# Performance work log

Hardware: AMD Instinct MI355X
Metric: run time of the kernel (lower is better)

Reference implementation:

```python
import jax, jax.numpy as jnp
import numpy as np
from jax import lax

B, T, D = 4, 1024, 1024
H = 16
HD = D // H
MIN_K, MAX_K = 3, 9
KS = (3, 5, 7, 9)  # candidate odd kernel sizes


def setup_inputs() -> dict:
    key = jax.random.key(0)
    ks = jax.random.split(key, 16)
    s = 0.02
    inp = {
        "x": jax.random.normal(ks[0], (B, T, D), jnp.float32),
        "Wq": jax.random.normal(ks[1], (D, D), jnp.float32) * s,
        "bq": jnp.zeros((D,), jnp.float32),
        "Wk": jax.random.normal(ks[2], (D, D), jnp.float32) * s,
        "bk": jnp.zeros((D,), jnp.float32),
        "Wv": jax.random.normal(ks[3], (D, D), jnp.float32) * s,
        "bv": jnp.zeros((D,), jnp.float32),
        # per-head Conv1d weights (H, out_ch=HD, in_ch=HD, MAX_K) and biases (H, HD)
        "conv_w": jax.random.normal(ks[4], (H, HD, HD, MAX_K), jnp.float32) * s,
        "conv_b": jax.random.normal(ks[5], (H, HD), jnp.float32) * s,
        # kernel_proj: Linear(1,16) -> ReLU -> Linear(16,1), stored as (in,out)
        "kp_w1": jax.random.normal(ks[6], (1, 16), jnp.float32) * 0.5,
        "kp_b1": jnp.zeros((16,), jnp.float32),
        "kp_w2": jax.random.normal(ks[7], (16, 1), jnp.float32) * 0.5,
        "kp_b2": jnp.zeros((1,), jnp.float32),
        "fc_w": jax.random.normal(ks[8], (D, D), jnp.float32) * s,
        "fc_b": jnp.zeros((D,), jnp.float32),
        "ln_g": jnp.ones((D,), jnp.float32),
        "ln_b": jnp.zeros((D,), jnp.float32),
    }
    return inp


def reference(x, Wq, bq, Wk, bk, Wv, bv, conv_w, conv_b,
              kp_w1, kp_b1, kp_w2, kp_b2, fc_w, fc_b, ln_g, ln_b):
    scale = HD ** -0.5
    q = (x @ Wq + bq).reshape(B, T, H, HD).transpose(0, 2, 1, 3)  # (B,H,T,HD)
    k = (x @ Wk + bk).reshape(B, T, H, HD).transpose(0, 2, 1, 3)
    v = (x @ Wv + bv).reshape(B, T, H, HD).transpose(0, 2, 1, 3)

    attn = jax.nn.softmax(jnp.einsum('bhqd,bhkd->bhqk', q, k) * scale, axis=-1)

    # head importance -> dynamic kernel size per head
    importance = attn.mean(axis=(-2, -1)).mean(axis=0)  # (H,)
    imp_norm = (importance - importance.min()) / (importance.max() - importance.min() + 1e-6)
    hmid = jax.nn.relu(imp_norm[:, None] @ kp_w1 + kp_b1)  # (H,16)
    frac = jax.nn.sigmoid((hmid @ kp_w2 + kp_b2)[:, 0])    # (H,)
    kv = jnp.round(MIN_K + frac * (MAX_K - MIN_K)).astype(jnp.int32)
    kv = kv + (1 - kv % 2)                                 # force odd
    kv = jnp.clip(kv, MIN_K, MAX_K)
    k_idx = jnp.clip((kv - MIN_K) // 2, 0, len(KS) - 1)    # (H,) candidate index

    out = jnp.einsum('bhqk,bhkd->bhqd', attn, v)           # (B,H,T,HD)
    out_c = out.transpose(0, 1, 3, 2).reshape(B, H * HD, T)  # NCH grouped layout

    center = MAX_K // 2
    cands = []
    for kk in KS:
        half = kk // 2
        w = conv_w[:, :, :, center - half:center + half + 1].reshape(H * HD, HD, kk)
        y = lax.conv_general_dilated(out_c, w, (1,), 'VALID',
                                     dimension_numbers=('NCH', 'OIH', 'NCH'),
                                     feature_group_count=H)
        y = y + conv_b.reshape(1, H * HD, 1)
        # smart edge-replication pad of conv OUTPUT back to length T
        y = jnp.pad(y, ((0, 0), (0, 0), (half, kk - 1 - half)), mode='edge')
        cands.append(y)
    cands = jnp.stack(cands).reshape(len(KS), B, H, HD, T)  # (K,B,H,HD,T)

    onehot = jax.nn.one_hot(k_idx, len(KS), dtype=cands.dtype)  # (H,K)
    sel = jnp.einsum('kbhdt,hk->bhdt', cands, onehot)           # (B,H,HD,T)
    out_cat = sel.transpose(0, 3, 1, 2).reshape(B, T, D)

    proj = out_cat @ fc_w + fc_b
    y = proj + x
    mu = y.mean(axis=-1, keepdims=True)
    var = ((y - mu) ** 2).mean(axis=-1, keepdims=True)
    return (y - mu) / jnp.sqrt(var + 1e-5) * ln_g + ln_b
```

## Files before the change

### kernel.cpp

```cpp
#include <hip/hip_runtime.h>
#include <math.h>

constexpr int Bn = 4, Tn = 1024, Dn = 1024, Hn = 16, HDn = 64;

typedef __attribute__((ext_vector_type(8))) short short8;
typedef __attribute__((ext_vector_type(4))) float floatx4;
typedef __attribute__((ext_vector_type(4))) unsigned short ushort4v;

static __device__ __forceinline__ unsigned short f2bf(float f) {
  union { float f; unsigned int u; } v; v.f = f;
  unsigned int u = v.u;
  unsigned int r = (u + 0x7fffu + ((u >> 16) & 1u)) >> 16;
  return (unsigned short)r;
}

static __device__ __forceinline__ float bf2f(unsigned short s) {
  union { unsigned int u; float f; } v;
  v.u = ((unsigned int)s) << 16;
  return v.f;
}

static __device__ __forceinline__ unsigned short f2bf_fast(float f) {
  union { float f; unsigned int u; } v; v.f = f;
  return (unsigned short)((v.u + 0x8000u) >> 16);
}

static __device__ __forceinline__ void gload_lds16(const void* g, void* l) {
  __builtin_amdgcn_global_load_lds(
      (const __attribute__((address_space(1))) unsigned int*)g,
      (__attribute__((address_space(3))) unsigned int*)l, 16, 0, 0);
}


__global__ __launch_bounds__(256) void prep_all(
    const float* __restrict__ X, unsigned short* __restrict__ Xb,
    const float* __restrict__ conv_w, unsigned short* __restrict__ Wc,
    const float* __restrict__ W0, const float* __restrict__ W1,
    const float* __restrict__ W2, const float* __restrict__ W3,
    unsigned short* __restrict__ O0, unsigned short* __restrict__ O1,
    unsigned short* __restrict__ O2, unsigned short* __restrict__ O3)
{
  const int tid = threadIdx.x;
  if (blockIdx.x < 4096) {
    int i = (blockIdx.x * 256 + tid) * 4;
    float4 v = *(const float4*)(X + i);
    ushort4v o;
    o.x = f2bf(v.x); o.y = f2bf(v.y); o.z = f2bf(v.z); o.w = f2bf(v.w);
    *(ushort4v*)(Xb + i) = o;
  } else if (blockIdx.x < 5888) {
    int idx = (blockIdx.x - 4096) * 256 + tid;
    int i = idx & 63;
    int o = (idx >> 6) & 63;
    int j = (idx >> 12) % 7;
    int h = idx / (7 * 4096);
    Wc[idx] = f2bf(conv_w[(((size_t)(h * 64 + o) * 64 + i) * 9) + 1 + j]);
  } else {
    int bid = blockIdx.x - 5888;
    int z = bid >> 8;
    int rem = bid & 255;
    int cx = rem & 15, ry = rem >> 4;
    const float* W = (z == 0) ? W0 : (z == 1) ? W1 : (z == 2) ? W2 : W3;
    unsigned short* O = (z == 0) ? O0 : (z == 1) ? O1 : (z == 2) ? O2 : O3;
    __shared__ float tile[64][65];
    const int c0 = cx * 64, r0 = ry * 64;
    for (int i = tid; i < 4096; i += 256) {
      int r = i >> 6, c = i & 63;
      tile[r][c] = W[(size_t)(r0 + r) * 1024 + c0 + c];
    }
    __syncthreads();
    for (int i = tid; i < 4096; i += 256) {
      int r = i >> 6, c = i & 63;
      O[(size_t)(c0 + r) * 1024 + r0 + c] = f2bf(tile[c][r]);
    }
  }
}

__global__ __launch_bounds__(256) void gemm_qkv_mfma(
    const unsigned short* __restrict__ Ab,
    const unsigned short* __restrict__ WqT, const unsigned short* __restrict__ WkT,
    const unsigned short* __restrict__ WvT,
    const float* __restrict__ bq, const float* __restrict__ bk, const float* __restrict__ bv,
    unsigned short* __restrict__ Qb, unsigned short* __restrict__ Kb,
    unsigned short* __restrict__ Vtb)
{
  __shared__ unsigned short As[128 * 64];
  __shared__ unsigned short Bs[128 * 64];
  const int tid = threadIdx.x;
  const int lane = tid & 63;
  const int ln = lane & 15, g = lane >> 4;
  const int wave = tid >> 6;
  const int wm = (wave >> 1) * 64, wn = (wave & 1) * 64;
  const int m0 = blockIdx.y * 128;
  const int ng = blockIdx.x * 128;
  const int which = ng >> 10;
  const int n0 = ng & 1023;
  const unsigned short* Wt = (which == 0) ? WqT : (which == 1) ? WkT : WvT;
  const float* bia = (which == 0) ? bq : (which == 1) ? bk : bv;

  const unsigned short* aSrc[4]; unsigned short* aDst[4];
  const unsigned short* bSrc[4]; unsigned short* bDst[4];
  #pragma unroll
  for (int it = 0; it < 4; ++it) {
    int L = it * 256 + tid;
    int r = L >> 3, sc = L & 7;
    int c = sc ^ (r & 7);
    aSrc[it] = Ab + (size_t)(m0 + r) * 1024 + c * 8;
    aDst[it] = As + L * 8;
    bSrc[it] = Wt + (size_t)(n0 + r) * 1024 + c * 8;
    bDst[it] = Bs + L * 8;
  }

  floatx4 acc[4][4];
  #pragma unroll
  for (int mt = 0; mt < 4; ++mt)
    #pragma unroll
    for (int nt = 0; nt < 4; ++nt) acc[mt][nt] = (floatx4)0.f;

  for (int k0 = 0; k0 < 1024; k0 += 64) {
    __syncthreads();
    #pragma unroll
    for (int it = 0; it < 4; ++it) {
      gload_lds16(aSrc[it] + k0, aDst[it]);
      gload_lds16(bSrc[it] + k0, bDst[it]);
    }
    __syncthreads();
    #pragma unroll
    for (int s = 0; s < 2; ++s) {
      short8 af[4], bf[4];
      #pragma unroll
      for (int mt = 0; mt < 4; ++mt) {
        int R = wm + mt * 16 + ln;
        int ch = (s * 4 + g) ^ (R & 7);
        af[mt] = *(const short8*)&As[(R * 8 + ch) * 8];
      }
      #pragma unroll
      for (int nt = 0; nt < 4; ++nt) {
        int R = wn + nt * 16 + ln;
        int ch = (s * 4 + g) ^ (R & 7);
        bf[nt] = *(const short8*)&Bs[(R * 8 + ch) * 8];
      }
      #pragma unroll
      for (int mt = 0; mt < 4; ++mt)
        #pragma unroll
        for (int nt = 0; nt < 4; ++nt)
          acc[mt][nt] = __builtin_amdgcn_mfma_f32_16x16x32_bf16(af[mt], bf[nt], acc[mt][nt], 0, 0, 0);
    }
  }

  const int b = m0 >> 10;
  const int tbase = m0 & 1023;
  #pragma unroll
  for (int nt = 0; nt < 4; ++nt) {
    int nl = wn + nt * 16 + ln;
    float bv_ = bia[n0 + nl];
    int h = (n0 + nl) >> 6, hd = (n0 + nl) & 63;
    #pragma unroll
    for (int mt = 0; mt < 4; ++mt) {
      int t = tbase + wm + mt * 16 + g * 4;
      if (which < 2) {
        unsigned short* Out = (which == 0) ? Qb : Kb;
        size_t base = (((size_t)b * Hn + h) * Tn + t) * HDn + hd;
        #pragma unroll
        for (int r = 0; r < 4; ++r)
          Out[base + (size_t)r * HDn] = f2bf(acc[mt][nt][r] + bv_);
      } else {
        ushort4v o;
        #pragma unroll
        for (int r = 0; r < 4; ++r) o[r] = f2bf(acc[mt][nt][r] + bv_);
        *(ushort4v*)(Vtb + (((size_t)b * Hn + h) * HDn + hd) * Tn + t) = o;
      }
    }
  }
}

__global__ __launch_bounds__(256) void gemm_fc_mfma(
    const unsigned short* __restrict__ Ab, const unsigned short* __restrict__ WT,
    const float* __restrict__ bia, unsigned short* __restrict__ PRb)
{
  __shared__ unsigned short As[128 * 64];
  __shared__ unsigned short Bs[128 * 64];
  const int tid = threadIdx.x;
  const int lane = tid & 63;
  const int ln = lane & 15, g = lane >> 4;
  const int wave = tid >> 6;
  const int wm = (wave >> 1) * 64, wn = (wave & 1) * 64;
  const int m0 = blockIdx.y * 128;
  const int n0 = blockIdx.x * 128;

  const unsigned short* aSrc[4]; unsigned short* aDst[4];
  const unsigned short* bSrc[4]; unsigned short* bDst[4];
  #pragma unroll
  for (int it = 0; it < 4; ++it) {
    int L = it * 256 + tid;
    int r = L >> 3, sc = L & 7;
    int c = sc ^ (r & 7);
    aSrc[it] = Ab + (size_t)(m0 + r) * 1024 + c * 8;
    aDst[it] = As + L * 8;
    bSrc[it] = WT + (size_t)(n0 + r) * 1024 + c * 8;
    bDst[it] = Bs + L * 8;
  }

  floatx4 acc[4][4];
  #pragma unroll
  for (int mt = 0; mt < 4; ++mt)
    #pragma unroll
    for (int nt = 0; nt < 4; ++nt) acc[mt][nt] = (floatx4)0.f;

  for (int k0 = 0; k0 < 1024; k0 += 64) {
    __syncthreads();
    #pragma unroll
    for (int it = 0; it < 4; ++it) {
      gload_lds16(aSrc[it] + k0, aDst[it]);
      gload_lds16(bSrc[it] + k0, bDst[it]);
    }
    __syncthreads();
    #pragma unroll
    for (int s = 0; s < 2; ++s) {
      short8 af[4], bf[4];
      #pragma unroll
      for (int mt = 0; mt < 4; ++mt) {
        int R = wm + mt * 16 + ln;
        int ch = (s * 4 + g) ^ (R & 7);
        af[mt] = *(const short8*)&As[(R * 8 + ch) * 8];
      }
      #pragma unroll
      for (int nt = 0; nt < 4; ++nt) {
        int R = wn + nt * 16 + ln;
        int ch = (s * 4 + g) ^ (R & 7);
        bf[nt] = *(const short8*)&Bs[(R * 8 + ch) * 8];
      }
      #pragma unroll
      for (int mt = 0; mt < 4; ++mt)
        #pragma unroll
        for (int nt = 0; nt < 4; ++nt)
          acc[mt][nt] = __builtin_amdgcn_mfma_f32_16x16x32_bf16(af[mt], bf[nt], acc[mt][nt], 0, 0, 0);
    }
  }

  #pragma unroll
  for (int nt = 0; nt < 4; ++nt) {
    int n = n0 + wn + nt * 16 + ln;
    float bv_ = bia[n];
    #pragma unroll
    for (int mt = 0; mt < 4; ++mt) {
      int m = m0 + wm + mt * 16 + g * 4;
      unsigned short* base = PRb + (size_t)m * Dn + n;
      #pragma unroll
      for (int r = 0; r < 4; ++r) base[(size_t)r * Dn] = f2bf(acc[mt][nt][r] + bv_);
    }
  }
}

__global__ __launch_bounds__(512) void attn_mfma(
    const unsigned short* __restrict__ Qb, const unsigned short* __restrict__ Kb,
    const unsigned short* __restrict__ Vtb, unsigned short* __restrict__ AO)
{
  __shared__ unsigned short Ks[64 * 64];
  __shared__ unsigned short Vts[64 * 64];
  __shared__ unsigned short Ps[128 * 72];

  const int bh = blockIdx.y;
  const int q0 = blockIdx.x * 128;
  const int tid = threadIdx.x;
  const int lane = tid & 63;
  const int ln = lane & 15;
  const int g  = lane >> 4;
  const int wq = (tid >> 6) * 16;

  const unsigned short* Kp  = Kb  + (size_t)bh * Tn * HDn;
  const unsigned short* Vtp = Vtb + (size_t)bh * HDn * Tn;

  const unsigned short* Qrow = Qb + ((size_t)bh * Tn + q0 + wq + ln) * HDn;
  short8 qa0 = *(const short8*)(Qrow + g * 8);
  short8 qa1 = *(const short8*)(Qrow + 32 + g * 8);

  const int r_ = tid >> 3, sc_ = tid & 7;
  const int c_ = sc_ ^ (r_ & 7);
  const unsigned short* kSrc = Kp + (size_t)r_ * HDn + c_ * 8;
  unsigned short* kDst = Ks + tid * 8;
  const unsigned short* vSrc = Vtp + (size_t)r_ * Tn + c_ * 8;
  unsigned short* vDst = Vts + tid * 8;

  floatx4 o[4];
  #pragma unroll
  for (int dt = 0; dt < 4; ++dt) o[dt] = (floatx4)0.f;
  float l[4] = {0.f, 0.f, 0.f, 0.f};

  constexpr float CEXP = 0.18033688011112042f;

  for (int kt = 0; kt < Tn; kt += 64) {
    __syncthreads();
    gload_lds16(kSrc + (size_t)kt * HDn, kDst);
    gload_lds16(vSrc + kt, vDst);
    __syncthreads();

    floatx4 s[4];
    #pragma unroll
    for (int nt = 0; nt < 4; ++nt) {
      int R = nt * 16 + ln;
      int ch0 = g ^ (ln & 7), ch1 = (4 + g) ^ (ln & 7);
      short8 kb0 = *(const short8*)&Ks[(R * 8 + ch0) * 8];
      short8 kb1 = *(const short8*)&Ks[(R * 8 + ch1) * 8];
      s[nt] = (floatx4)0.f;
      s[nt] = __builtin_amdgcn_mfma_f32_16x16x32_bf16(qa0, kb0, s[nt], 0, 0, 0);
      s[nt] = __builtin_amdgcn_mfma_f32_16x16x32_bf16(qa1, kb1, s[nt], 0, 0, 0);
    }

    #pragma unroll
    for (int r = 0; r < 4; ++r) {
      #pragma unroll
      for (int nt = 0; nt < 4; ++nt) {
        float pv = __builtin_amdgcn_exp2f(s[nt][r] * CEXP);
        l[r] += pv;
        Ps[(wq + g * 4 + r) * 72 + nt * 16 + ln] = f2bf_fast(pv);
      }
    }

    short8 pa0 = *(const short8*)&Ps[(wq + ln) * 72 + g * 8];
    short8 pa1 = *(const short8*)&Ps[(wq + ln) * 72 + 32 + g * 8];

    #pragma unroll
    for (int dt = 0; dt < 4; ++dt) {
      int R = dt * 16 + ln;
      int ch0 = g ^ (ln & 7), ch1 = (4 + g) ^ (ln & 7);
      short8 vb0 = *(const short8*)&Vts[(R * 8 + ch0) * 8];
      short8 vb1 = *(const short8*)&Vts[(R * 8 + ch1) * 8];
      o[dt] = __builtin_amdgcn_mfma_f32_16x16x32_bf16(pa0, vb0, o[dt], 0, 0, 0);
      o[dt] = __builtin_amdgcn_mfma_f32_16x16x32_bf16(pa1, vb1, o[dt], 0, 0, 0);
    }
  }

  float inv[4];
  #pragma unroll
  for (int r = 0; r < 4; ++r) {
    float rs = l[r];
    rs += __shfl_xor(rs, 1);
    rs += __shfl_xor(rs, 2);
    rs += __shfl_xor(rs, 4);
    rs += __shfl_xor(rs, 8);
    inv[r] = 1.f / rs;
  }
  unsigned short* Op = AO + ((size_t)bh * Tn + q0 + wq) * HDn;
  #pragma unroll
  for (int dt = 0; dt < 4; ++dt)
    #pragma unroll
    for (int r = 0; r < 4; ++r)
      Op[(size_t)(g * 4 + r) * HDn + dt * 16 + ln] = f2bf(o[dt][r] * inv[r]);
}

__global__ __launch_bounds__(256) void conv_mfma(
    const unsigned short* __restrict__ Xb, const unsigned short* __restrict__ Wc,
    const float* __restrict__ conv_b, unsigned short* __restrict__ CO)
{
  __shared__ unsigned short Wl[7 * 32 * 64];
  __shared__ unsigned short Xs[134 * 64];
  const int tid = threadIdx.x;
  const int lane = tid & 63;
  const int ln = lane & 15, g = lane >> 4;
  const int wave = tid >> 6;
  const int wm = wave * 32;
  const int t0 = blockIdx.x * 128;
  const int o0 = blockIdx.y * 32;
  const int bh = blockIdx.z;
  const int b = bh >> 4, h = bh & 15;
  const unsigned short* Xp = Xb + (size_t)bh * Tn * HDn;
  const unsigned short* Wp = Wc + ((size_t)h * 7 * 64 + o0) * 64;

  #pragma unroll
  for (int it = 0; it < 7; ++it) {
    int L = it * 256 + tid;
    int row = L >> 3, sc = L & 7;
    int c = sc ^ (row & 7);
    int j = row >> 5, ol = row & 31;
    gload_lds16(Wp + ((size_t)j * 64 + ol) * 64 + c * 8, Wl + L * 8);
  }
  #pragma unroll
  for (int it = 0; it < 5; ++it) {
    int L = it * 256 + tid;
    if (L < 134 * 8) {
      int lr = L >> 3, sc = L & 7;
      int c = sc ^ (lr & 7);
      int gr = min(max(t0 - 3 + lr, 0), Tn - 1);
      gload_lds16(Xp + (size_t)gr * HDn + c * 8, Xs + L * 8);
    }
  }
  __syncthreads();

  floatx4 acc[2][2];
  #pragma unroll
  for (int mt = 0; mt < 2; ++mt)
    #pragma unroll
    for (int nt = 0; nt < 2; ++nt) acc[mt][nt] = (floatx4)0.f;

  int tb[2];
  #pragma unroll
  for (int mt = 0; mt < 2; ++mt)
    tb[mt] = min(max(t0 + wm + mt * 16 + ln, 3), Tn - 4) - t0;

  #pragma unroll
  for (int j = 0; j < 7; ++j) {
    #pragma unroll
    for (int s = 0; s < 2; ++s) {
      short8 af[2], bf[2];
      #pragma unroll
      for (int mt = 0; mt < 2; ++mt) {
        int lr = tb[mt] + j;
        int ch = (s * 4 + g) ^ (lr & 7);
        af[mt] = *(const short8*)&Xs[lr * 64 + ch * 8];
      }
      #pragma unroll
      for (int nt = 0; nt < 2; ++nt) {
        int row = j * 32 + nt * 16 + ln;
        int ch = (s * 4 + g) ^ (row & 7);
        bf[nt] = *(const short8*)&Wl[row * 64 + ch * 8];
      }
      #pragma unroll
      for (int mt = 0; mt < 2; ++mt)
        #pragma unroll
        for (int nt = 0; nt < 2; ++nt)
          acc[mt][nt] = __builtin_amdgcn_mfma_f32_16x16x32_bf16(af[mt], bf[nt], acc[mt][nt], 0, 0, 0);
    }
  }

  #pragma unroll
  for (int nt = 0; nt < 2; ++nt) {
    int o = o0 + nt * 16 + ln;
    float bias = conv_b[(h << 6) + o];
    #pragma unroll
    for (int mt = 0; mt < 2; ++mt) {
      int t = t0 + wm + mt * 16 + g * 4;
      #pragma unroll
      for (int r = 0; r < 4; ++r)
        CO[((size_t)b * Tn + t + r) * Dn + (h << 6) + o] = f2bf(acc[mt][nt][r] + bias);
    }
  }
}

__global__ __launch_bounds__(256) void res_ln(
    const unsigned short* __restrict__ Pb, const float* __restrict__ Xin,
    const float* __restrict__ g, const float* __restrict__ be,
    float* __restrict__ Out)
{
  const int r = blockIdx.x;
  const int tid = threadIdx.x;
  const int c = tid * 4;
  ushort4v pv4 = *(const ushort4v*)(Pb + (size_t)r * Dn + c);
  float4 xv = *(const float4*)(Xin + (size_t)r * Dn + c);
  float v0 = bf2f(pv4.x) + xv.x, v1 = bf2f(pv4.y) + xv.y;
  float v2 = bf2f(pv4.z) + xv.z, v3 = bf2f(pv4.w) + xv.w;
  float s = v0 + v1 + v2 + v3;
  float s2 = v0 * v0 + v1 * v1 + v2 * v2 + v3 * v3;
  #pragma unroll
  for (int off = 32; off > 0; off >>= 1) {
    s += __shfl_down(s, off);
    s2 += __shfl_down(s2, off);
  }
  __shared__ float rs[4], rs2[4];
  __shared__ float smu, srstd;
  const int wid = tid >> 6;
  if ((tid & 63) == 0) { rs[wid] = s; rs2[wid] = s2; }
  __syncthreads();
  if (tid == 0) {
    float S = rs[0] + rs[1] + rs[2] + rs[3];
    float S2 = rs2[0] + rs2[1] + rs2[2] + rs2[3];
    float mu = S * (1.f / Dn);
    float var = S2 * (1.f / Dn) - mu * mu;
    smu = mu;
    srstd = rsqrtf(var + 1e-5f);
  }
  __syncthreads();
  float mu = smu, rstd = srstd;
  float4 gv = *(const float4*)(g + c);
  float4 bv = *(const float4*)(be + c);
  float4 ov;
  ov.x = (v0 - mu) * rstd * gv.x + bv.x;
  ov.y = (v1 - mu) * rstd * gv.y + bv.y;
  ov.z = (v2 - mu) * rstd * gv.z + bv.z;
  ov.w = (v3 - mu) * rstd * gv.w + bv.w;
  *(float4*)(Out + (size_t)r * Dn + c) = ov;
}

extern "C" void kernel_launch(void* const* d_in, const int* in_sizes, int n_in,
                              void* d_out, int out_size, void* d_ws, size_t ws_size,
                              hipStream_t stream) {
  const float* x      = (const float*)d_in[0];
  const float* Wq     = (const float*)d_in[1];
  const float* bq     = (const float*)d_in[2];
  const float* Wk     = (const float*)d_in[3];
  const float* bk     = (const float*)d_in[4];
  const float* Wv     = (const float*)d_in[5];
  const float* bv     = (const float*)d_in[6];
  const float* conv_w = (const float*)d_in[7];
  const float* conv_b = (const float*)d_in[8];
  const float* fc_w   = (const float*)d_in[13];
  const float* fc_b   = (const float*)d_in[14];
  const float* ln_g   = (const float*)d_in[15];
  const float* ln_b   = (const float*)d_in[16];
  float* out = (float*)d_out;

  unsigned char* w8 = (unsigned char*)d_ws;
  const size_t MB = 1024 * 1024;
  unsigned short* Xb  = (unsigned short*)(w8);
  unsigned short* WqT = (unsigned short*)(w8 + 8 * MB);
  unsigned short* WkT = (unsigned short*)(w8 + 10 * MB);
  unsigned short* WvT = (unsigned short*)(w8 + 12 * MB);
  unsigned short* fcT = (unsigned short*)(w8 + 14 * MB);
  unsigned short* Qb  = (unsigned short*)(w8 + 16 * MB);
  unsigned short* Kb  = (unsigned short*)(w8 + 24 * MB);
  unsigned short* Vtb = (unsigned short*)(w8 + 32 * MB);
  unsigned short* AO  = (unsigned short*)(w8 + 40 * MB);
  unsigned short* Wc  = (unsigned short*)(w8 + 48 * MB);
  unsigned short* CO  = (unsigned short*)(w8);
  unsigned short* PRb = (unsigned short*)(w8 + 16 * MB);

  prep_all<<<dim3(6912), 256, 0, stream>>>(x, Xb, conv_w, Wc,
                                           Wq, Wk, Wv, fc_w, WqT, WkT, WvT, fcT);
  gemm_qkv_mfma<<<dim3(24, 32), 256, 0, stream>>>(Xb, WqT, WkT, WvT, bq, bk, bv, Qb, Kb, Vtb);
  attn_mfma<<<dim3(8, 64), 512, 0, stream>>>(Qb, Kb, Vtb, AO);
  conv_mfma<<<dim3(8, 2, 64), 256, 0, stream>>>(AO, Wc, conv_b, CO);
  gemm_fc_mfma<<<dim3(8, 32), 256, 0, stream>>>(CO, fcT, fc_b, PRb);
  res_ln<<<dim3(Bn * Tn), 256, 0, stream>>>(PRb, x, ln_g, ln_b, out);
}
```

Before: 221.6 us.

## Double-buffer LDS tiles with register prefetch in GEMMs and attention

Replaces the direct global-to-LDS loads in the QKV GEMM, FC GEMM and attention kernels with a register-staged, double-buffered scheme. The next K-tile is loaded into registers before the MFMA work on the current tile and written to the alternate LDS buffer afterwards, so each iteration needs one barrier instead of two. This aims to hide global memory latency behind compute. In exchange it doubles LDS use per block, which may lower occupancy, and adds register pressure from the staging registers.

```diff
diff --git a/kernel.cpp b/kernel.cpp
--- a/kernel.cpp
+++ b/kernel.cpp
@@ -23,12 +23,6 @@
 static __device__ __forceinline__ unsigned short f2bf_fast(float f) {
   union { float f; unsigned int u; } v; v.f = f;
   return (unsigned short)((v.u + 0x8000u) >> 16);
-}
-
-static __device__ __forceinline__ void gload_lds16(const void* g, void* l) {
-  __builtin_amdgcn_global_load_lds(
-      (const __attribute__((address_space(1))) unsigned int*)g,
-      (__attribute__((address_space(3))) unsigned int*)l, 16, 0, 0);
 }
 
 
@@ -83,8 +77,8 @@
     unsigned short* __restrict__ Qb, unsigned short* __restrict__ Kb,
     unsigned short* __restrict__ Vtb)
 {
-  __shared__ unsigned short As[128 * 64];
-  __shared__ unsigned short Bs[128 * 64];
+  __shared__ unsigned short As[2][128 * 64];
+  __shared__ unsigned short Bs[2][128 * 64];
   const int tid = threadIdx.x;
   const int lane = tid & 63;
   const int ln = lane & 15, g = lane >> 4;
@@ -97,18 +91,31 @@
   const unsigned short* Wt = (which == 0) ? WqT : (which == 1) ? WkT : WvT;
   const float* bia = (which == 0) ? bq : (which == 1) ? bk : bv;
 
-  const unsigned short* aSrc[4]; unsigned short* aDst[4];
-  const unsigned short* bSrc[4]; unsigned short* bDst[4];
+  const unsigned short* aSrc[4];
+  const unsigned short* bSrc[4];
+  int dOff[4];
   #pragma unroll
   for (int it = 0; it < 4; ++it) {
     int L = it * 256 + tid;
     int r = L >> 3, sc = L & 7;
     int c = sc ^ (r & 7);
     aSrc[it] = Ab + (size_t)(m0 + r) * 1024 + c * 8;
-    aDst[it] = As + L * 8;
     bSrc[it] = Wt + (size_t)(n0 + r) * 1024 + c * 8;
-    bDst[it] = Bs + L * 8;
-  }
+    dOff[it] = L * 8;
+  }
+
+  short8 aR[4], bR[4];
+  #pragma unroll
+  for (int it = 0; it < 4; ++it) {
+    aR[it] = *(const short8*)(aSrc[it]);
+    bR[it] = *(const short8*)(bSrc[it]);
+  }
+  #pragma unroll
+  for (int it = 0; it < 4; ++it) {
+    *(short8*)&As[0][dOff[it]] = aR[it];
+    *(short8*)&Bs[0][dOff[it]] = bR[it];
+  }
+  __syncthreads();
 
   floatx4 acc[4][4];
   #pragma unroll
@@ -116,14 +123,16 @@
     #pragma unroll
     for (int nt = 0; nt < 4; ++nt) acc[mt][nt] = (floatx4)0.f;
 
+  int p = 0;
   for (int k0 = 0; k0 < 1024; k0 += 64) {
-    __syncthreads();
-    #pragma unroll
-    for (int it = 0; it < 4; ++it) {
-      gload_lds16(aSrc[it] + k0, aDst[it]);
-      gload_lds16(bSrc[it] + k0, bDst[it]);
-    }
-    __syncthreads();
+    const bool more = (k0 + 64) < 1024;
+    if (more) {
+      #pragma unroll
+      for (int it = 0; it < 4; ++it) {
+        aR[it] = *(const short8*)(aSrc[it] + k0 + 64);
+        bR[it] = *(const short8*)(bSrc[it] + k0 + 64);
+      }
+    }
     #pragma unroll
     for (int s = 0; s < 2; ++s) {
       short8 af[4], bf[4];
@@ -131,13 +140,13 @@
       for (int mt = 0; mt < 4; ++mt) {
         int R = wm + mt * 16 + ln;
         int ch = (s * 4 + g) ^ (R & 7);
-        af[mt] = *(const short8*)&As[(R * 8 + ch) * 8];
+        af[mt] = *(const short8*)&As[p][(R * 8 + ch) * 8];
       }
       #pragma unroll
       for (int nt = 0; nt < 4; ++nt) {
         int R = wn + nt * 16 + ln;
         int ch = (s * 4 + g) ^ (R & 7);
-        bf[nt] = *(const short8*)&Bs[(R * 8 + ch) * 8];
+        bf[nt] = *(const short8*)&Bs[p][(R * 8 + ch) * 8];
       }
       #pragma unroll
       for (int mt = 0; mt < 4; ++mt)
@@ -145,6 +154,16 @@
         for (int nt = 0; nt < 4; ++nt)
           acc[mt][nt] = __builtin_amdgcn_mfma_f32_16x16x32_bf16(af[mt], bf[nt], acc[mt][nt], 0, 0, 0);
     }
+    if (more) {
+      const int np = p ^ 1;
+      #pragma unroll
+      for (int it = 0; it < 4; ++it) {
+        *(short8*)&As[np][dOff[it]] = aR[it];
+        *(short8*)&Bs[np][dOff[it]] = bR[it];
+      }
+    }
+    __syncthreads();
+    p ^= 1;
   }
 
   const int b = m0 >> 10;
@@ -177,8 +196,8 @@
     const unsigned short* __restrict__ Ab, const unsigned short* __restrict__ WT,
     const float* __restrict__ bia, unsigned short* __restrict__ PRb)
 {
-  __shared__ unsigned short As[128 * 64];
-  __shared__ unsigned short Bs[128 * 64];
+  __shared__ unsigned short As[2][128 * 64];
+  __shared__ unsigned short Bs[2][128 * 64];
   const int tid = threadIdx.x;
   const int lane = tid & 63;
   const int ln = lane & 15, g = lane >> 4;
@@ -187,18 +206,31 @@
   const int m0 = blockIdx.y * 128;
   const int n0 = blockIdx.x * 128;
 
-  const unsigned short* aSrc[4]; unsigned short* aDst[4];
-  const unsigned short* bSrc[4]; unsigned short* bDst[4];
+  const unsigned short* aSrc[4];
+  const unsigned short* bSrc[4];
+  int dOff[4];
   #pragma unroll
   for (int it = 0; it < 4; ++it) {
     int L = it * 256 + tid;
     int r = L >> 3, sc = L & 7;
     int c = sc ^ (r & 7);
     aSrc[it] = Ab + (size_t)(m0 + r) * 1024 + c * 8;
-    aDst[it] = As + L * 8;
     bSrc[it] = WT + (size_t)(n0 + r) * 1024 + c * 8;
-    bDst[it] = Bs + L * 8;
-  }
+    dOff[it] = L * 8;
+  }
+
+  short8 aR[4], bR[4];
+  #pragma unroll
+  for (int it = 0; it < 4; ++it) {
+    aR[it] = *(const short8*)(aSrc[it]);
+    bR[it] = *(const short8*)(bSrc[it]);
+  }
+  #pragma unroll
+  for (int it = 0; it < 4; ++it) {
+    *(short8*)&As[0][dOff[it]] = aR[it];
+    *(short8*)&Bs[0][dOff[it]] = bR[it];
+  }
+  __syncthreads();
 
   floatx4 acc[4][4];
   #pragma unroll
@@ -206,14 +238,16 @@
     #pragma unroll
     for (int nt = 0; nt < 4; ++nt) acc[mt][nt] = (floatx4)0.f;
 
+  int p = 0;
   for (int k0 = 0; k0 < 1024; k0 += 64) {
-    __syncthreads();
-    #pragma unroll
-    for (int it = 0; it < 4; ++it) {
-      gload_lds16(aSrc[it] + k0, aDst[it]);
-      gload_lds16(bSrc[it] + k0, bDst[it]);
-    }
-    __syncthreads();
+    const bool more = (k0 + 64) < 1024;
+    if (more) {
+      #pragma unroll
+      for (int it = 0; it < 4; ++it) {
+        aR[it] = *(const short8*)(aSrc[it] + k0 + 64);
+        bR[it] = *(const short8*)(bSrc[it] + k0 + 64);
+      }
+    }
     #pragma unroll
     for (int s = 0; s < 2; ++s) {
       short8 af[4], bf[4];
@@ -221,13 +255,13 @@
       for (int mt = 0; mt < 4; ++mt) {
         int R = wm + mt * 16 + ln;
         int ch = (s * 4 + g) ^ (R & 7);
-        af[mt] = *(const short8*)&As[(R * 8 + ch) * 8];
+        af[mt] = *(const short8*)&As[p][(R * 8 + ch) * 8];
       }
       #pragma unroll
       for (int nt = 0; nt < 4; ++nt) {
         int R = wn + nt * 16 + ln;
         int ch = (s * 4 + g) ^ (R & 7);
-        bf[nt] = *(const short8*)&Bs[(R * 8 + ch) * 8];
+        bf[nt] = *(const short8*)&Bs[p][(R * 8 + ch) * 8];
       }
       #pragma unroll
       for (int mt = 0; mt < 4; ++mt)
@@ -235,6 +269,16 @@
         for (int nt = 0; nt < 4; ++nt)
           acc[mt][nt] = __builtin_amdgcn_mfma_f32_16x16x32_bf16(af[mt], bf[nt], acc[mt][nt], 0, 0, 0);
     }
+    if (more) {
+      const int np = p ^ 1;
+      #pragma unroll
+      for (int it = 0; it < 4; ++it) {
+        *(short8*)&As[np][dOff[it]] = aR[it];
+        *(short8*)&Bs[np][dOff[it]] = bR[it];
+      }
+    }
+    __syncthreads();
+    p ^= 1;
   }
 
   #pragma unroll
@@ -255,8 +299,8 @@
     const unsigned short* __restrict__ Qb, const unsigned short* __restrict__ Kb,
     const unsigned short* __restrict__ Vtb, unsigned short* __restrict__ AO)
 {
-  __shared__ unsigned short Ks[64 * 64];
-  __shared__ unsigned short Vts[64 * 64];
+  __shared__ unsigned short Ks[2][64 * 64];
+  __shared__ unsigned short Vts[2][64 * 64];
   __shared__ unsigned short Ps[128 * 72];
 
   const int bh = blockIdx.y;
@@ -277,9 +321,14 @@
   const int r_ = tid >> 3, sc_ = tid & 7;
   const int c_ = sc_ ^ (r_ & 7);
   const unsigned short* kSrc = Kp + (size_t)r_ * HDn + c_ * 8;
-  unsigned short* kDst = Ks + tid * 8;
   const unsigned short* vSrc = Vtp + (size_t)r_ * Tn + c_ * 8;
-  unsigned short* vDst = Vts + tid * 8;
+  const int dO = tid * 8;
+
+  short8 kR = *(const short8*)(kSrc);
+  short8 vR = *(const short8*)(vSrc);
+  *(short8*)&Ks[0][dO] = kR;
+  *(short8*)&Vts[0][dO] = vR;
+  __syncthreads();
 
   floatx4 o[4];
   #pragma unroll
@@ -288,19 +337,21 @@
 
   constexpr float CEXP = 0.18033688011112042f;
 
+  int p = 0;
   for (int kt = 0; kt < Tn; kt += 64) {
-    __syncthreads();
-    gload_lds16(kSrc + (size_t)kt * HDn, kDst);
-    gload_lds16(vSrc + kt, vDst);
-    __syncthreads();
+    const bool more = (kt + 64) < Tn;
+    if (more) {
+      kR = *(const short8*)(kSrc + (size_t)(kt + 64) * HDn);
+      vR = *(const short8*)(vSrc + kt + 64);
+    }
 
     floatx4 s[4];
     #pragma unroll
     for (int nt = 0; nt < 4; ++nt) {
       int R = nt * 16 + ln;
       int ch0 = g ^ (ln & 7), ch1 = (4 + g) ^ (ln & 7);
-      short8 kb0 = *(const short8*)&Ks[(R * 8 + ch0) * 8];
-      short8 kb1 = *(const short8*)&Ks[(R * 8 + ch1) * 8];
+      short8 kb0 = *(const short8*)&Ks[p][(R * 8 + ch0) * 8];
+      short8 kb1 = *(const short8*)&Ks[p][(R * 8 + ch1) * 8];
       s[nt] = (floatx4)0.f;
       s[nt] = __builtin_amdgcn_mfma_f32_16x16x32_bf16(qa0, kb0, s[nt], 0, 0, 0);
       s[nt] = __builtin_amdgcn_mfma_f32_16x16x32_bf16(qa1, kb1, s[nt], 0, 0, 0);
@@ -323,11 +374,19 @@
     for (int dt = 0; dt < 4; ++dt) {
       int R = dt * 16 + ln;
       int ch0 = g ^ (ln & 7), ch1 = (4 + g) ^ (ln & 7);
-      short8 vb0 = *(const short8*)&Vts[(R * 8 + ch0) * 8];
-      short8 vb1 = *(const short8*)&Vts[(R * 8 + ch1) * 8];
+      short8 vb0 = *(const short8*)&Vts[p][(R * 8 + ch0) * 8];
+      short8 vb1 = *(const short8*)&Vts[p][(R * 8 + ch1) * 8];
       o[dt] = __builtin_amdgcn_mfma_f32_16x16x32_bf16(pa0, vb0, o[dt], 0, 0, 0);
       o[dt] = __builtin_amdgcn_mfma_f32_16x16x32_bf16(pa1, vb1, o[dt], 0, 0, 0);
     }
+
+    if (more) {
+      const int np = p ^ 1;
+      *(short8*)&Ks[np][dO] = kR;
+      *(short8*)&Vts[np][dO] = vR;
+    }
+    __syncthreads();
+    p ^= 1;
   }
 
   float inv[4];
@@ -346,6 +405,12 @@
     #pragma unroll
     for (int r = 0; r < 4; ++r)
       Op[(size_t)(g * 4 + r) * HDn + dt * 16 + ln] = f2bf(o[dt][r] * inv[r]);
+}
+
+static __device__ __forceinline__ void gload_lds16(const void* g, void* l) {
+  __builtin_amdgcn_global_load_lds(
+      (const __attribute__((address_space(1))) unsigned int*)g,
+      (__attribute__((address_space(3))) unsigned int*)l, 16, 0, 0);
 }
 
 __global__ __launch_bounds__(256) void conv_mfma(
```

Result: no change. 219.1 us (-1.1%).
